# Kernel tuning notes

Hardware: AMD Instinct MI355X
Metric: run time of the kernel (lower is better)

## Reference

```python
import jax, jax.numpy as jnp
import numpy as np

B, C_IN, C_OUT = 2, 32, 32
N_IN = 128 * 128            # input grid points
N_OUT = 128 * 128           # output grid points
KERNEL_SIZE = 9             # (3-1)*4 + 1 for kernel_shape=[3,4], piecewise_linear basis
NNZ = 1_500_000             # sparse entries in psi (kernel_size, n_out, n_in)


def setup_inputs() -> dict:
    key = jax.random.key(0)
    ks = jax.random.split(key, 8)
    scale = (1.0 / C_IN) ** 0.5  # sqrt(1/groupsize), groups=1
    return {
        "x": jax.random.normal(ks[0], (B, C_IN, N_IN), jnp.float32),
        "quadrature_weights": jax.random.uniform(ks[1], (N_IN,), jnp.float32, 0.5, 1.5) / N_IN,
        "psi_vals": jax.random.uniform(ks[2], (NNZ,), jnp.float32),
        "weight": scale * jax.random.normal(ks[3], (C_OUT, C_IN, KERNEL_SIZE), jnp.float32),
        "bias": jnp.zeros((C_OUT,), jnp.float32),
        "psi_idx_k": jax.random.randint(ks[4], (NNZ,), 0, KERNEL_SIZE, dtype=jnp.int32),
        "psi_idx_out": jax.random.randint(ks[5], (NNZ,), 0, N_OUT, dtype=jnp.int32),
        "psi_idx_in": jax.random.randint(ks[6], (NNZ,), 0, N_IN, dtype=jnp.int32),
        "n_out": N_OUT,
    }


def reference(x, quadrature_weights, psi_vals, weight, bias,
              psi_idx_k, psi_idx_out, psi_idx_in, n_out):
    # x: (B, C, n_in); weight: (O, C, K); psi is sparse (K, n_out, n_in)
    Bb, C, n_in = x.shape
    K = weight.shape[2]
    # pre-multiply by quadrature weights, layout (n_in, B, C) for gather
    xq = (x * quadrature_weights[None, None, :]).transpose(2, 0, 1)
    # gather-weight: contribution of each sparse entry  -> (nnz, B, C)
    contrib = xq[psi_idx_in] * psi_vals[:, None, None]
    # scatter-add into (kernel, out) bins == sparse psi @ xq
    seg = psi_idx_k * n_out + psi_idx_out
    xk = jax.ops.segment_sum(contrib, seg, num_segments=K * n_out)
    xk = xk.reshape(K, n_out, Bb, C)  # (K, n_out, B, C)
    # channel/kernel mixing with learned weight (groups=1)
    out = jnp.einsum("knbc,ock->bon", xk, weight) + bias[None, :, None]
    return out  # (B, out_channels, n_out)
```

## Files before the change

kernel.cpp:

```cpp
#include <hip/hip_runtime.h>

#define N_IN   16384
#define N_OUT  16384
#define KSZ    9
#define CIN    32
#define COUT   32
#define BC     64
#define NCB    256
#define CHA    4096
#define ECAP_A 8192
#define ROWS   144
#define XSTR   68
#define SCAP   2048

union PrepSH {
    struct { int cnt[NCB]; int cntE[NCB]; int gbase[NCB]; int cursor[NCB];
             float2 slist[CHA]; } bin;
    struct { float tile[64 * 65]; } xqp;
};

__global__ __launch_bounds__(512) void k_prep(
        const float* __restrict__ x, const float* __restrict__ qw,
        const float* __restrict__ vals, const float* __restrict__ w,
        const int* __restrict__ ik, const int* __restrict__ io,
        const int* __restrict__ ii, float* __restrict__ xq,
        float2* __restrict__ sivA, int* __restrict__ gcntA,
        float* __restrict__ wT, int nnz, int nchA) {
    __shared__ PrepSH sh;
    const int t = threadIdx.x;
    const int bid = blockIdx.x;

    if (bid >= nchA) {
        if (bid < nchA + 256) {
            const int in0 = (bid - nchA) * 64;
#pragma unroll
            for (int i = 0; i < 8; ++i) {
                int idx = t + i * 512;
                int bcl = idx >> 6, inl = idx & 63;
                sh.xqp.tile[bcl * 65 + inl] = x[bcl * N_IN + in0 + inl];
            }
            __syncthreads();
#pragma unroll
            for (int i = 0; i < 8; ++i) {
                int idx = t + i * 512;
                int inl = idx >> 6, bcl = idx & 63;
                xq[(size_t)(in0 + inl) * BC + bcl] = sh.xqp.tile[bcl * 65 + inl] * qw[in0 + inl];
            }
        } else {
            for (int i = t; i < COUT * CIN * KSZ; i += 512) {
                int o = i / (CIN * KSZ);
                int r = i - o * (CIN * KSZ);
                int c = r / KSZ;
                int k = r - c * KSZ;
                wT[((k * 8 + (o >> 2)) * 32 + c) * 4 + (o & 3)] = w[i];
            }
        }
        return;
    }

    if (t < NCB) sh.bin.cnt[t] = 0;
    __syncthreads();
    const int base = bid * CHA;
    const int e0   = base + t * 8;

    float vv[8]; int pk[8]; int bk[8]; bool hv[8];
    if (e0 + 8 <= nnz) {
        int4 a0 = *(const int4*)(io + e0),  a1 = *(const int4*)(io + e0 + 4);
        int4 b0 = *(const int4*)(ii + e0),  b1 = *(const int4*)(ii + e0 + 4);
        int4 k0 = *(const int4*)(ik + e0),  k1 = *(const int4*)(ik + e0 + 4);
        float4 d0 = *(const float4*)(vals + e0), d1 = *(const float4*)(vals + e0 + 4);
        int ov[8] = {a0.x, a0.y, a0.z, a0.w, a1.x, a1.y, a1.z, a1.w};
        int iv[8] = {b0.x, b0.y, b0.z, b0.w, b1.x, b1.y, b1.z, b1.w};
        int kv[8] = {k0.x, k0.y, k0.z, k0.w, k1.x, k1.y, k1.z, k1.w};
        float dv[8] = {d0.x, d0.y, d0.z, d0.w, d1.x, d1.y, d1.z, d1.w};
#pragma unroll
        for (int j = 0; j < 8; ++j) {
            hv[j] = true;
            bk[j] = ov[j] >> 6;
            pk[j] = (int)(((unsigned)(ov[j] >> 4) << 22)) | (iv[j] << 8) | (kv[j] * 16 + (ov[j] & 15));
            vv[j] = dv[j];
        }
    } else {
#pragma unroll
        for (int j = 0; j < 8; ++j) {
            int e = e0 + j;
            hv[j] = (e < nnz);
            if (hv[j]) {
                int o = io[e];
                bk[j] = o >> 6;
                pk[j] = (int)(((unsigned)(o >> 4) << 22)) | (ii[e] << 8) | (ik[e] * 16 + (o & 15));
                vv[j] = vals[e];
            } else { bk[j] = 0; pk[j] = 0; vv[j] = 0.f; }
        }
    }
#pragma unroll
    for (int j = 0; j < 8; ++j) if (hv[j]) atomicAdd(&sh.bin.cnt[bk[j]], 1);
    __syncthreads();
    if (t < NCB) {
        int cv = sh.bin.cnt[t];
        sh.bin.gbase[t] = t * ECAP_A + (cv ? atomicAdd(&gcntA[t], cv) : 0);
    }
    if (t < 64) {
        int carry = 0;
#pragma unroll
        for (int seg = 0; seg < 4; ++seg) {
            int idx = seg * 64 + t;
            int v = sh.bin.cnt[idx];
            int orig = v;
#pragma unroll
            for (int off = 1; off < 64; off <<= 1) {
                int u = __shfl_up(v, off);
                if (t >= off) v += u;
            }
            sh.bin.cntE[idx]   = carry + v - orig;
            sh.bin.cursor[idx] = carry + v - orig;
            carry += __shfl(v, 63);
        }
    }
    __syncthreads();
#pragma unroll
    for (int j = 0; j < 8; ++j) {
        if (hv[j]) {
            int pos = atomicAdd(&sh.bin.cursor[bk[j]], 1);
            sh.bin.slist[pos] = make_float2(vv[j], __int_as_float(pk[j]));
        }
    }
    __syncthreads();
    const int m = min(nnz - base, CHA);
    for (int p = t; p < m; p += 512) {
        float2 f2 = sh.bin.slist[p];
        int cb = (int)((unsigned)__float_as_int(f2.y) >> 24);
        int dest = sh.bin.gbase[cb] + (p - sh.bin.cntE[cb]);
        if (dest < (cb + 1) * ECAP_A) sivA[dest] = f2;
    }
}

__global__ __launch_bounds__(512) void k_fused6(const float* __restrict__ xq,
        const float2* __restrict__ sivA, const int* __restrict__ gcntA,
        const float* __restrict__ wT, const float* __restrict__ bias,
        float* __restrict__ out) {
    __shared__ __align__(16) float sxk[80 * XSTR];
    __shared__ float2 slist[SCAP];
    __shared__ int    rowStart[ROWS + 1];
    __shared__ int    cursor[ROWS];
    __shared__ int    mcur;
    const int tid  = threadIdx.x;
    const int lane = tid & 63;
    const int wv   = __builtin_amdgcn_readfirstlane(tid >> 6);
    const unsigned f = blockIdx.x;

    if (tid < ROWS) rowStart[tid] = 0;
    if (tid == 0) mcur = 0;
    __syncthreads();

    const int cb = (int)(f >> 2);
    const int mA = min(gcntA[cb], ECAP_A);
    const float2* src = sivA + (size_t)cb * ECAP_A;
    float2* tmp = (float2*)sxk;
    for (int i = tid; i < mA; i += 512) {
        float2 v = src[i];
        unsigned fid = (unsigned)__float_as_int(v.y) >> 22;
        if (fid == f) {
            int pos = atomicAdd(&mcur, 1);
            if (pos < SCAP) {
                tmp[pos] = v;
                atomicAdd(&rowStart[__float_as_int(v.y) & 0xFF], 1);
            }
        }
    }
    __syncthreads();
    const int m2 = min(mcur, SCAP);
    if (wv == 0) {
        int carry = 0;
#pragma unroll
        for (int i0 = 0; i0 < 192; i0 += 64) {
            int idx = i0 + lane;
            int v = (idx < ROWS) ? rowStart[idx] : 0;
            int orig = v;
#pragma unroll
            for (int off = 1; off < 64; off <<= 1) {
                int u = __shfl_up(v, off);
                if (lane >= off) v += u;
            }
            if (idx < ROWS) {
                int excl = carry + v - orig;
                rowStart[idx] = excl;
                cursor[idx]   = excl;
            }
            carry += __shfl(v, 63);
        }
        if (lane == 0) rowStart[ROWS] = carry;
    }
    __syncthreads();
    for (int i = tid; i < m2; i += 512) {
        float2 v = tmp[i];
        int p = __float_as_int(v.y);
        int pos = atomicAdd(&cursor[p & 0xFF], 1);
        slist[pos] = make_float2(v.x, __int_as_float(p & 0x3FFF00));
    }
    __syncthreads();

    const char* xqb   = (const char*)xq;
    const int   lane4 = lane * 4;
    const int   h     = lane >> 4;
    const int   nl    = lane & 15;
    float acc[4] = {0.f, 0.f, 0.f, 0.f};

#pragma unroll
    for (int ph = 0; ph < 2; ++ph) {
        const int rbase = ph ? 80 : 0;
        const int rend  = ph ? 144 : 80;
        const int nrows = rend - rbase;
        for (int i = tid; i < nrows * XSTR; i += 512) sxk[i] = 0.f;
        __syncthreads();
        for (int r = rbase + wv; r < rend; r += 8) {
            const int a = rowStart[r], b = rowStart[r + 1];
            if (a >= b) continue;
            float acc0 = 0.f, acc1 = 0.f, acc2 = 0.f, acc3 = 0.f;
            int i = a;
            for (; i + 7 < b; i += 8) {
                float2 v0 = slist[i],     v1 = slist[i + 1], v2 = slist[i + 2], v3 = slist[i + 3];
                float2 v4 = slist[i + 4], v5 = slist[i + 5], v6 = slist[i + 6], v7 = slist[i + 7];
                acc0 += *(const float*)(xqb + (__float_as_int(v0.y) + lane4)) * v0.x;
                acc1 += *(const float*)(xqb + (__float_as_int(v1.y) + lane4)) * v1.x;
                acc2 += *(const float*)(xqb + (__float_as_int(v2.y) + lane4)) * v2.x;
                acc3 += *(const float*)(xqb + (__float_as_int(v3.y) + lane4)) * v3.x;
                acc0 += *(const float*)(xqb + (__float_as_int(v4.y) + lane4)) * v4.x;
                acc1 += *(const float*)(xqb + (__float_as_int(v5.y) + lane4)) * v5.x;
                acc2 += *(const float*)(xqb + (__float_as_int(v6.y) + lane4)) * v6.x;
                acc3 += *(const float*)(xqb + (__float_as_int(v7.y) + lane4)) * v7.x;
            }
            for (; i + 3 < b; i += 4) {
                float2 v0 = slist[i], v1 = slist[i + 1], v2 = slist[i + 2], v3 = slist[i + 3];
                acc0 += *(const float*)(xqb + (__float_as_int(v0.y) + lane4)) * v0.x;
                acc1 += *(const float*)(xqb + (__float_as_int(v1.y) + lane4)) * v1.x;
                acc2 += *(const float*)(xqb + (__float_as_int(v2.y) + lane4)) * v2.x;
                acc3 += *(const float*)(xqb + (__float_as_int(v3.y) + lane4)) * v3.x;
            }
            for (; i < b; ++i) {
                float2 v = slist[i];
                acc0 += *(const float*)(xqb + (__float_as_int(v.y) + lane4)) * v.x;
            }
            sxk[(r - rbase) * XSTR + lane] = (acc0 + acc1) + (acc2 + acc3);
        }
        __syncthreads();
        if (lane < 32) {
            const int kbase = ph ? 5 : 0;
            const int kcnt  = ph ? 4 : 5;
            for (int kk = 0; kk < kcnt; ++kk) {
                const float* xr = &sxk[(kk * 16 + nl) * XSTR + h * 32];
                const float* wp = &wT[((kbase + kk) * 8 + wv) * 128];
#pragma unroll
                for (int c4 = 0; c4 < 8; ++c4) {
                    float4 xv = *(const float4*)&xr[c4 * 4];
#pragma unroll
                    for (int cc = 0; cc < 4; ++cc) {
                        float xval = (&xv.x)[cc];
#pragma unroll
                        for (int j = 0; j < 4; ++j)
                            acc[j] += xval * wp[(c4 * 4 + cc) * 4 + j];
                    }
                }
            }
        }
        __syncthreads();
    }

    if (lane < 32) {
        const int n0 = (int)f * 16;
#pragma unroll
        for (int j = 0; j < 4; ++j) {
            int o = wv * 4 + j;
            out[((size_t)h * COUT + o) * N_OUT + n0 + nl] = acc[j] + bias[o];
        }
    }
}

extern "C" void kernel_launch(void* const* d_in, const int* in_sizes, int n_in,
                              void* d_out, int out_size, void* d_ws, size_t ws_size,
                              hipStream_t stream) {
    const float* x    = (const float*)d_in[0];
    const float* qw   = (const float*)d_in[1];
    const float* vals = (const float*)d_in[2];
    const float* w    = (const float*)d_in[3];
    const float* bias = (const float*)d_in[4];
    const int*   ik   = (const int*)d_in[5];
    const int*   io   = (const int*)d_in[6];
    const int*   ii   = (const int*)d_in[7];
    const int    nnz  = in_sizes[2];
    const int    nchA = (nnz + CHA - 1) / CHA;

    char* ws = (char*)d_ws;
    float*  xq    = (float*)ws;  ws += (size_t)N_IN * BC * 4;
    float2* sivA  = (float2*)ws; ws += (size_t)NCB * ECAP_A * 8;
    int*    gcntA = (int*)ws;    ws += NCB * 4;
    float*  wT    = (float*)ws;  ws += (size_t)COUT * CIN * KSZ * 4;

    hipMemsetAsync(gcntA, 0, NCB * sizeof(int), stream);
    k_prep  <<<nchA + 257, 512, 0, stream>>>(x, qw, vals, w, ik, io, ii,
                                             xq, sivA, gcntA, wT, nnz, nchA);
    k_fused6<<<1024, 512, 0, stream>>>(xq, sivA, gcntA, wT, bias, (float*)d_out);
}
```

Measured before the change: 149.2 us.

## Bin sparse entries directly per 32-output tile and use 1024-thread fused blocks

The prep kernel now bins entries into 512 buckets of 32 output points each, so every fused block reads only its own bucket. Before, four blocks each scanned a shared 64-point bucket and filtered out the entries that were not theirs. The fused kernel runs 512 blocks of 1024 threads, processes 288 rows in three phases of 96, and splits the channel-mixing work across all 16 waves. The aim is to remove the redundant bucket scanning and the temporary compaction pass, and to keep more lanes busy during mixing. The trade-off is fewer blocks overall and tighter capacity clamping per bucket (4096 entries, against an average of about 2900).

After: 297.8 us. 2x slower.

```diff
diff --git a/kernel.cpp b/kernel.cpp
--- a/kernel.cpp
+++ b/kernel.cpp
@@ -6,16 +6,16 @@
 #define CIN    32
 #define COUT   32
 #define BC     64
-#define NCB    256
+#define NCB    512
 #define CHA    4096
-#define ECAP_A 8192
-#define ROWS   144
+#define ECAP_F 4096
+#define ROWS   288
+#define PHROWS 96
 #define XSTR   68
-#define SCAP   2048
 
 union PrepSH {
     struct { int cnt[NCB]; int cntE[NCB]; int gbase[NCB]; int cursor[NCB];
-             float2 slist[CHA]; } bin;
+             int segsum[8]; float2 slist[CHA]; } bin;
     struct { float tile[64 * 65]; } xqp;
 };
 
@@ -24,7 +24,7 @@
         const float* __restrict__ vals, const float* __restrict__ w,
         const int* __restrict__ ik, const int* __restrict__ io,
         const int* __restrict__ ii, float* __restrict__ xq,
-        float2* __restrict__ sivA, int* __restrict__ gcntA,
+        float2* __restrict__ sivF, int* __restrict__ gcntF,
         float* __restrict__ wT, int nnz, int nchA) {
     __shared__ PrepSH sh;
     const int t = threadIdx.x;
@@ -58,7 +58,7 @@
         return;
     }
 
-    if (t < NCB) sh.bin.cnt[t] = 0;
+    sh.bin.cnt[t] = 0;
     __syncthreads();
     const int base = bid * CHA;
     const int e0   = base + t * 8;
@@ -76,8 +76,8 @@
 #pragma unroll
         for (int j = 0; j < 8; ++j) {
             hv[j] = true;
-            bk[j] = ov[j] >> 6;
-            pk[j] = (int)(((unsigned)(ov[j] >> 4) << 22)) | (iv[j] << 8) | (kv[j] * 16 + (ov[j] & 15));
+            bk[j] = ov[j] >> 5;
+            pk[j] = (int)(((unsigned)(ov[j] >> 5)) << 23) | (iv[j] << 9) | (kv[j] * 32 + (ov[j] & 31));
             vv[j] = dv[j];
         }
     } else {
@@ -87,8 +87,8 @@
             hv[j] = (e < nnz);
             if (hv[j]) {
                 int o = io[e];
-                bk[j] = o >> 6;
-                pk[j] = (int)(((unsigned)(o >> 4) << 22)) | (ii[e] << 8) | (ik[e] * 16 + (o & 15));
+                bk[j] = o >> 5;
+                pk[j] = (int)(((unsigned)(o >> 5)) << 23) | (ii[e] << 9) | (ik[e] * 32 + (o & 31));
                 vv[j] = vals[e];
             } else { bk[j] = 0; pk[j] = 0; vv[j] = 0.f; }
         }
@@ -96,27 +96,28 @@
 #pragma unroll
     for (int j = 0; j < 8; ++j) if (hv[j]) atomicAdd(&sh.bin.cnt[bk[j]], 1);
     __syncthreads();
-    if (t < NCB) {
-        int cv = sh.bin.cnt[t];
-        sh.bin.gbase[t] = t * ECAP_A + (cv ? atomicAdd(&gcntA[t], cv) : 0);
-    }
-    if (t < 64) {
-        int carry = 0;
-#pragma unroll
-        for (int seg = 0; seg < 4; ++seg) {
-            int idx = seg * 64 + t;
-            int v = sh.bin.cnt[idx];
-            int orig = v;
-#pragma unroll
-            for (int off = 1; off < 64; off <<= 1) {
-                int u = __shfl_up(v, off);
-                if (t >= off) v += u;
-            }
-            sh.bin.cntE[idx]   = carry + v - orig;
-            sh.bin.cursor[idx] = carry + v - orig;
-            carry += __shfl(v, 63);
-        }
-    }
+
+    const int lane = t & 63;
+    const int wvp  = t >> 6;
+    const int cv = sh.bin.cnt[t];
+    sh.bin.gbase[t] = t * ECAP_F + (cv ? atomicAdd(&gcntF[t], cv) : 0);
+    int v = cv;
+#pragma unroll
+    for (int off = 1; off < 64; off <<= 1) {
+        int u = __shfl_up(v, off);
+        if (lane >= off) v += u;
+    }
+    if (lane == 63) sh.bin.segsum[wvp] = v;
+    __syncthreads();
+    if (t == 0) {
+        int c = 0;
+#pragma unroll
+        for (int s = 0; s < 8; ++s) { int xs = sh.bin.segsum[s]; sh.bin.segsum[s] = c; c += xs; }
+    }
+    __syncthreads();
+    const int excl = v - cv + sh.bin.segsum[wvp];
+    sh.bin.cntE[t]   = excl;
+    sh.bin.cursor[t] = excl;
     __syncthreads();
 #pragma unroll
     for (int j = 0; j < 8; ++j) {
@@ -129,51 +130,39 @@
     const int m = min(nnz - base, CHA);
     for (int p = t; p < m; p += 512) {
         float2 f2 = sh.bin.slist[p];
-        int cb = (int)((unsigned)__float_as_int(f2.y) >> 24);
+        int cb = (int)((unsigned)__float_as_int(f2.y) >> 23);
         int dest = sh.bin.gbase[cb] + (p - sh.bin.cntE[cb]);
-        if (dest < (cb + 1) * ECAP_A) sivA[dest] = f2;
+        if (dest < (cb + 1) * ECAP_F) sivF[dest] = f2;
     }
 }
 
-__global__ __launch_bounds__(512) void k_fused6(const float* __restrict__ xq,
-        const float2* __restrict__ sivA, const int* __restrict__ gcntA,
+__global__ __launch_bounds__(1024, 8) void k_fused7(const float* __restrict__ xq,
+        const float2* __restrict__ sivF, const int* __restrict__ gcntF,
         const float* __restrict__ wT, const float* __restrict__ bias,
         float* __restrict__ out) {
-    __shared__ __align__(16) float sxk[80 * XSTR];
-    __shared__ float2 slist[SCAP];
-    __shared__ int    rowStart[ROWS + 1];
-    __shared__ int    cursor[ROWS];
-    __shared__ int    mcur;
+    __shared__ __align__(16) float sxk[PHROWS * XSTR];
+    __shared__ __align__(16) float2 slist[ECAP_F];
+    __shared__ int rowStart[ROWS + 1];
+    __shared__ int cursor[ROWS];
     const int tid  = threadIdx.x;
     const int lane = tid & 63;
     const int wv   = __builtin_amdgcn_readfirstlane(tid >> 6);
     const unsigned f = blockIdx.x;
 
     if (tid < ROWS) rowStart[tid] = 0;
-    if (tid == 0) mcur = 0;
-    __syncthreads();
-
-    const int cb = (int)(f >> 2);
-    const int mA = min(gcntA[cb], ECAP_A);
-    const float2* src = sivA + (size_t)cb * ECAP_A;
-    float2* tmp = (float2*)sxk;
-    for (int i = tid; i < mA; i += 512) {
-        float2 v = src[i];
-        unsigned fid = (unsigned)__float_as_int(v.y) >> 22;
-        if (fid == f) {
-            int pos = atomicAdd(&mcur, 1);
-            if (pos < SCAP) {
-                tmp[pos] = v;
-                atomicAdd(&rowStart[__float_as_int(v.y) & 0xFF], 1);
-            }
-        }
-    }
-    __syncthreads();
-    const int m2 = min(mcur, SCAP);
+    __syncthreads();
+
+    const int mF = min(gcntF[f], ECAP_F);
+    const float2* __restrict__ src = sivF + (size_t)f * ECAP_F;
+    const int* __restrict__ srcI = (const int*)src;
+    for (int i = tid; i < mF; i += 1024)
+        atomicAdd(&rowStart[srcI[2 * i + 1] & 0x1FF], 1);
+    __syncthreads();
+
     if (wv == 0) {
         int carry = 0;
 #pragma unroll
-        for (int i0 = 0; i0 < 192; i0 += 64) {
+        for (int i0 = 0; i0 < 320; i0 += 64) {
             int idx = i0 + lane;
             int v = (idx < ROWS) ? rowStart[idx] : 0;
             int orig = v;
@@ -192,30 +181,28 @@
         if (lane == 0) rowStart[ROWS] = carry;
     }
     __syncthreads();
-    for (int i = tid; i < m2; i += 512) {
-        float2 v = tmp[i];
+
+    for (int i = tid; i < mF; i += 1024) {
+        float2 v = src[i];
         int p = __float_as_int(v.y);
-        int pos = atomicAdd(&cursor[p & 0xFF], 1);
-        slist[pos] = make_float2(v.x, __int_as_float(p & 0x3FFF00));
+        int pos = atomicAdd(&cursor[p & 0x1FF], 1);
+        slist[pos] = make_float2(v.x, __int_as_float((p >> 1) & 0x3FFF00));
     }
     __syncthreads();
 
     const char* xqb   = (const char*)xq;
     const int   lane4 = lane * 4;
-    const int   h     = lane >> 4;
-    const int   nl    = lane & 15;
-    float acc[4] = {0.f, 0.f, 0.f, 0.f};
-
-#pragma unroll
-    for (int ph = 0; ph < 2; ++ph) {
-        const int rbase = ph ? 80 : 0;
-        const int rend  = ph ? 144 : 80;
-        const int nrows = rend - rbase;
-        for (int i = tid; i < nrows * XSTR; i += 512) sxk[i] = 0.f;
-        __syncthreads();
-        for (int r = rbase + wv; r < rend; r += 8) {
+    const int   b_    = lane >> 5;
+    const int   n32   = lane & 31;
+    const int   oq    = wv >> 1;
+    const int   ol    = (wv & 1) * 2;
+    float acc[2] = {0.f, 0.f};
+
+#pragma unroll
+    for (int ph = 0; ph < 3; ++ph) {
+        const int rbase = ph * PHROWS;
+        for (int r = rbase + wv; r < rbase + PHROWS; r += 16) {
             const int a = rowStart[r], b = rowStart[r + 1];
-            if (a >= b) continue;
             float acc0 = 0.f, acc1 = 0.f, acc2 = 0.f, acc3 = 0.f;
             int i = a;
             for (; i + 7 < b; i += 8) {
@@ -244,35 +231,30 @@
             sxk[(r - rbase) * XSTR + lane] = (acc0 + acc1) + (acc2 + acc3);
         }
         __syncthreads();
-        if (lane < 32) {
-            const int kbase = ph ? 5 : 0;
-            const int kcnt  = ph ? 4 : 5;
-            for (int kk = 0; kk < kcnt; ++kk) {
-                const float* xr = &sxk[(kk * 16 + nl) * XSTR + h * 32];
-                const float* wp = &wT[((kbase + kk) * 8 + wv) * 128];
-#pragma unroll
-                for (int c4 = 0; c4 < 8; ++c4) {
-                    float4 xv = *(const float4*)&xr[c4 * 4];
-#pragma unroll
-                    for (int cc = 0; cc < 4; ++cc) {
-                        float xval = (&xv.x)[cc];
-#pragma unroll
-                        for (int j = 0; j < 4; ++j)
-                            acc[j] += xval * wp[(c4 * 4 + cc) * 4 + j];
-                    }
+        const int kbase = ph * 3;
+#pragma unroll
+        for (int kk = 0; kk < 3; ++kk) {
+            const float* xr = &sxk[(kk * 32 + n32) * XSTR + b_ * 32];
+            const float* wp = &wT[((kbase + kk) * 8 + oq) * 128 + ol];
+#pragma unroll
+            for (int c4 = 0; c4 < 8; ++c4) {
+                float4 xv = *(const float4*)&xr[c4 * 4];
+#pragma unroll
+                for (int cc = 0; cc < 4; ++cc) {
+                    float xval = (&xv.x)[cc];
+                    acc[0] += xval * wp[(c4 * 4 + cc) * 4];
+                    acc[1] += xval * wp[(c4 * 4 + cc) * 4 + 1];
                 }
             }
         }
         __syncthreads();
     }
 
-    if (lane < 32) {
-        const int n0 = (int)f * 16;
-#pragma unroll
-        for (int j = 0; j < 4; ++j) {
-            int o = wv * 4 + j;
-            out[((size_t)h * COUT + o) * N_OUT + n0 + nl] = acc[j] + bias[o];
-        }
+    const int n0 = (int)f * 32;
+#pragma unroll
+    for (int j = 0; j < 2; ++j) {
+        int o = oq * 4 + ol + j;
+        out[((size_t)b_ * COUT + o) * N_OUT + n0 + n32] = acc[j] + bias[o];
     }
 }
 
@@ -292,12 +274,12 @@
 
     char* ws = (char*)d_ws;
     float*  xq    = (float*)ws;  ws += (size_t)N_IN * BC * 4;
-    float2* sivA  = (float2*)ws; ws += (size_t)NCB * ECAP_A * 8;
-    int*    gcntA = (int*)ws;    ws += NCB * 4;
+    float2* sivF  = (float2*)ws; ws += (size_t)NCB * ECAP_F * 8;
+    int*    gcntF = (int*)ws;    ws += NCB * 4;
     float*  wT    = (float*)ws;  ws += (size_t)COUT * CIN * KSZ * 4;
 
-    hipMemsetAsync(gcntA, 0, NCB * sizeof(int), stream);
+    hipMemsetAsync(gcntF, 0, NCB * sizeof(int), stream);
     k_prep  <<<nchA + 257, 512, 0, stream>>>(x, qw, vals, w, ik, io, ii,
-                                             xq, sivA, gcntA, wT, nnz, nchA);
-    k_fused6<<<1024, 512, 0, stream>>>(xq, sivA, gcntA, wT, bias, (float*)d_out);
+                                             xq, sivF, gcntF, wT, nnz, nchA);
+    k_fused7<<<NCB, 1024, 0, stream>>>(xq, sivF, gcntF, wT, bias, (float*)d_out);
 }
```

## Bin sparse entries directly per output block to skip second-stage filtering

Applied to the files above, without the earlier changes.

The prep kernel now buckets entries into 1024 fine bins, one per consumer block, instead of 256 coarse bins. Each fused block therefore reads only its own entries. Before, it scanned a whole coarse bin of about 4x more data and filtered by block id with a shared atomic cursor. The global bin counters are padded with a stride of 16 to spread atomic contention. This trades a larger shared-memory histogram and a two-level scan in prep for a cheaper fused kernel, and it uses a tighter per-bin capacity that overflow could exceed.

Result: slower. 174.0 us (+16.7%).

```diff
diff --git a/kernel.cpp b/kernel.cpp
--- a/kernel.cpp
+++ b/kernel.cpp
@@ -6,16 +6,16 @@
 #define CIN    32
 #define COUT   32
 #define BC     64
-#define NCB    256
+#define NCB    1024
 #define CHA    4096
-#define ECAP_A 8192
+#define ECAP_F 2048
+#define GSTR   16
 #define ROWS   144
 #define XSTR   68
-#define SCAP   2048
 
 union PrepSH {
     struct { int cnt[NCB]; int cntE[NCB]; int gbase[NCB]; int cursor[NCB];
-             float2 slist[CHA]; } bin;
+             int segsum[8]; float2 slist[CHA]; } bin;
     struct { float tile[64 * 65]; } xqp;
 };
 
@@ -24,7 +24,7 @@
         const float* __restrict__ vals, const float* __restrict__ w,
         const int* __restrict__ ik, const int* __restrict__ io,
         const int* __restrict__ ii, float* __restrict__ xq,
-        float2* __restrict__ sivA, int* __restrict__ gcntA,
+        float2* __restrict__ sivF, int* __restrict__ gcntF,
         float* __restrict__ wT, int nnz, int nchA) {
     __shared__ PrepSH sh;
     const int t = threadIdx.x;
@@ -58,7 +58,8 @@
         return;
     }
 
-    if (t < NCB) sh.bin.cnt[t] = 0;
+    sh.bin.cnt[t] = 0;
+    sh.bin.cnt[t + 512] = 0;
     __syncthreads();
     const int base = bid * CHA;
     const int e0   = base + t * 8;
@@ -76,7 +77,7 @@
 #pragma unroll
         for (int j = 0; j < 8; ++j) {
             hv[j] = true;
-            bk[j] = ov[j] >> 6;
+            bk[j] = ov[j] >> 4;
             pk[j] = (int)(((unsigned)(ov[j] >> 4) << 22)) | (iv[j] << 8) | (kv[j] * 16 + (ov[j] & 15));
             vv[j] = dv[j];
         }
@@ -87,7 +88,7 @@
             hv[j] = (e < nnz);
             if (hv[j]) {
                 int o = io[e];
-                bk[j] = o >> 6;
+                bk[j] = o >> 4;
                 pk[j] = (int)(((unsigned)(o >> 4) << 22)) | (ii[e] << 8) | (ik[e] * 16 + (o & 15));
                 vv[j] = vals[e];
             } else { bk[j] = 0; pk[j] = 0; vv[j] = 0.f; }
@@ -96,26 +97,42 @@
 #pragma unroll
     for (int j = 0; j < 8; ++j) if (hv[j]) atomicAdd(&sh.bin.cnt[bk[j]], 1);
     __syncthreads();
-    if (t < NCB) {
-        int cv = sh.bin.cnt[t];
-        sh.bin.gbase[t] = t * ECAP_A + (cv ? atomicAdd(&gcntA[t], cv) : 0);
-    }
-    if (t < 64) {
+
+    const int lane = t & 63;
+    const int wvp  = t >> 6;
+    int cvv[2], exclv[2];
+    {
         int carry = 0;
 #pragma unroll
-        for (int seg = 0; seg < 4; ++seg) {
-            int idx = seg * 64 + t;
-            int v = sh.bin.cnt[idx];
-            int orig = v;
+        for (int s = 0; s < 2; ++s) {
+            const int idx = wvp * 128 + s * 64 + lane;
+            const int cv = sh.bin.cnt[idx];
+            cvv[s] = cv;
+            sh.bin.gbase[idx] = idx * ECAP_F + (cv ? atomicAdd(&gcntF[idx * GSTR], cv) : 0);
+            int v = cv;
 #pragma unroll
             for (int off = 1; off < 64; off <<= 1) {
                 int u = __shfl_up(v, off);
-                if (t >= off) v += u;
-            }
-            sh.bin.cntE[idx]   = carry + v - orig;
-            sh.bin.cursor[idx] = carry + v - orig;
+                if (lane >= off) v += u;
+            }
+            exclv[s] = carry + v - cv;
             carry += __shfl(v, 63);
         }
+        if (lane == 0) sh.bin.segsum[wvp] = carry;
+    }
+    __syncthreads();
+    if (t == 0) {
+        int c = 0;
+#pragma unroll
+        for (int s = 0; s < 8; ++s) { int xs = sh.bin.segsum[s]; sh.bin.segsum[s] = c; c += xs; }
+    }
+    __syncthreads();
+#pragma unroll
+    for (int s = 0; s < 2; ++s) {
+        const int idx = wvp * 128 + s * 64 + lane;
+        const int e = exclv[s] + sh.bin.segsum[wvp];
+        sh.bin.cntE[idx]   = e;
+        sh.bin.cursor[idx] = e;
     }
     __syncthreads();
 #pragma unroll
@@ -129,47 +146,35 @@
     const int m = min(nnz - base, CHA);
     for (int p = t; p < m; p += 512) {
         float2 f2 = sh.bin.slist[p];
-        int cb = (int)((unsigned)__float_as_int(f2.y) >> 24);
+        int cb = (int)((unsigned)__float_as_int(f2.y) >> 22);
         int dest = sh.bin.gbase[cb] + (p - sh.bin.cntE[cb]);
-        if (dest < (cb + 1) * ECAP_A) sivA[dest] = f2;
+        if (dest < (cb + 1) * ECAP_F) sivF[dest] = f2;
     }
 }
 
-__global__ __launch_bounds__(512) void k_fused6(const float* __restrict__ xq,
-        const float2* __restrict__ sivA, const int* __restrict__ gcntA,
+__global__ __launch_bounds__(512) void k_fused8(const float* __restrict__ xq,
+        const float2* __restrict__ sivF, const int* __restrict__ gcntF,
         const float* __restrict__ wT, const float* __restrict__ bias,
         float* __restrict__ out) {
     __shared__ __align__(16) float sxk[80 * XSTR];
-    __shared__ float2 slist[SCAP];
+    __shared__ __align__(16) float2 slist[ECAP_F];
     __shared__ int    rowStart[ROWS + 1];
     __shared__ int    cursor[ROWS];
-    __shared__ int    mcur;
     const int tid  = threadIdx.x;
     const int lane = tid & 63;
     const int wv   = __builtin_amdgcn_readfirstlane(tid >> 6);
     const unsigned f = blockIdx.x;
 
     if (tid < ROWS) rowStart[tid] = 0;
-    if (tid == 0) mcur = 0;
-    __syncthreads();
-
-    const int cb = (int)(f >> 2);
-    const int mA = min(gcntA[cb], ECAP_A);
-    const float2* src = sivA + (size_t)cb * ECAP_A;
-    float2* tmp = (float2*)sxk;
-    for (int i = tid; i < mA; i += 512) {
-        float2 v = src[i];
-        unsigned fid = (unsigned)__float_as_int(v.y) >> 22;
-        if (fid == f) {
-            int pos = atomicAdd(&mcur, 1);
-            if (pos < SCAP) {
-                tmp[pos] = v;
-                atomicAdd(&rowStart[__float_as_int(v.y) & 0xFF], 1);
-            }
-        }
-    }
-    __syncthreads();
-    const int m2 = min(mcur, SCAP);
+    __syncthreads();
+
+    const int mF = min(gcntF[f * GSTR], ECAP_F);
+    const float2* __restrict__ src = sivF + (size_t)f * ECAP_F;
+    const int* __restrict__ srcI = (const int*)src;
+    for (int i = tid; i < mF; i += 512)
+        atomicAdd(&rowStart[srcI[2 * i + 1] & 0xFF], 1);
+    __syncthreads();
+
     if (wv == 0) {
         int carry = 0;
 #pragma unroll
@@ -192,8 +197,8 @@
         if (lane == 0) rowStart[ROWS] = carry;
     }
     __syncthreads();
-    for (int i = tid; i < m2; i += 512) {
-        float2 v = tmp[i];
+    for (int i = tid; i < mF; i += 512) {
+        float2 v = src[i];
         int p = __float_as_int(v.y);
         int pos = atomicAdd(&cursor[p & 0xFF], 1);
         slist[pos] = make_float2(v.x, __int_as_float(p & 0x3FFF00));
@@ -292,12 +297,12 @@
 
     char* ws = (char*)d_ws;
     float*  xq    = (float*)ws;  ws += (size_t)N_IN * BC * 4;
-    float2* sivA  = (float2*)ws; ws += (size_t)NCB * ECAP_A * 8;
-    int*    gcntA = (int*)ws;    ws += NCB * 4;
+    float2* sivF  = (float2*)ws; ws += (size_t)NCB * ECAP_F * 8;
+    int*    gcntF = (int*)ws;    ws += (size_t)NCB * GSTR * 4;
     float*  wT    = (float*)ws;  ws += (size_t)COUT * CIN * KSZ * 4;
 
-    hipMemsetAsync(gcntA, 0, NCB * sizeof(int), stream);
+    hipMemsetAsync(gcntF, 0, (size_t)NCB * GSTR * sizeof(int), stream);
     k_prep  <<<nchA + 257, 512, 0, stream>>>(x, qw, vals, w, ik, io, ii,
-                                             xq, sivA, gcntA, wT, nnz, nchA);
-    k_fused6<<<1024, 512, 0, stream>>>(xq, sivA, gcntA, wT, bias, (float*)d_out);
+                                             xq, sivF, gcntF, wT, nnz, nchA);
+    k_fused8<<<NCB, 512, 0, stream>>>(xq, sivF, gcntF, wT, bias, (float*)d_out);
 }
```

## Merge four output-tile blocks per bin and overlap gather with mixing via double buffering

Applied to the files above, without the earlier changes.

The second kernel now launches one 1024-thread block per coarse bin instead of four 512-thread blocks that each rescanned the same bin's entries. Each entry is read once, kept in registers, bucketed by tile and row, and sorted into a larger shared list, which removes the redundant global reads and filtering. Work is then split across waves: half the waves gather the next half-tile of rows into one of two shared buffers while the other half run the channel/kernel mixing on the current buffer. In exchange the grid shrinks to 256 blocks, which may underfill the GPU, and shared memory per block grows substantially.

Result: slower. 177.2 us (+18.8%).

```diff
diff --git a/kernel.cpp b/kernel.cpp
--- a/kernel.cpp
+++ b/kernel.cpp
@@ -9,9 +9,8 @@
 #define NCB    256
 #define CHA    4096
 #define ECAP_A 8192
-#define ROWS   144
+#define ROWS4  576
 #define XSTR   68
-#define SCAP   2048
 
 union PrepSH {
     struct { int cnt[NCB]; int cntE[NCB]; int gbase[NCB]; int cursor[NCB];
@@ -135,68 +134,68 @@
     }
 }
 
-__global__ __launch_bounds__(512) void k_fused6(const float* __restrict__ xq,
+__global__ __launch_bounds__(1024) void k_fused10(const float* __restrict__ xq,
         const float2* __restrict__ sivA, const int* __restrict__ gcntA,
         const float* __restrict__ wT, const float* __restrict__ bias,
         float* __restrict__ out) {
-    __shared__ __align__(16) float sxk[80 * XSTR];
-    __shared__ float2 slist[SCAP];
-    __shared__ int    rowStart[ROWS + 1];
-    __shared__ int    cursor[ROWS];
-    __shared__ int    mcur;
+    __shared__ __align__(16) float sxk[2 * 80 * XSTR];
+    __shared__ __align__(16) float2 slist[ECAP_A];
+    __shared__ int rowStart[ROWS4 + 1];
+    __shared__ int cursor[ROWS4];
     const int tid  = threadIdx.x;
     const int lane = tid & 63;
     const int wv   = __builtin_amdgcn_readfirstlane(tid >> 6);
-    const unsigned f = blockIdx.x;
-
-    if (tid < ROWS) rowStart[tid] = 0;
-    if (tid == 0) mcur = 0;
-    __syncthreads();
-
-    const int cb = (int)(f >> 2);
+    const int cb   = blockIdx.x;
+
+    for (int i = tid; i < ROWS4; i += 1024) rowStart[i] = 0;
+    __syncthreads();
+
     const int mA = min(gcntA[cb], ECAP_A);
-    const float2* src = sivA + (size_t)cb * ECAP_A;
-    float2* tmp = (float2*)sxk;
-    for (int i = tid; i < mA; i += 512) {
-        float2 v = src[i];
-        unsigned fid = (unsigned)__float_as_int(v.y) >> 22;
-        if (fid == f) {
-            int pos = atomicAdd(&mcur, 1);
-            if (pos < SCAP) {
-                tmp[pos] = v;
-                atomicAdd(&rowStart[__float_as_int(v.y) & 0xFF], 1);
-            }
-        }
-    }
-    __syncthreads();
-    const int m2 = min(mcur, SCAP);
+    const float2* __restrict__ src = sivA + (size_t)cb * ECAP_A;
+
+    float2 rv[8];
+#pragma unroll
+    for (int j = 0; j < 8; ++j) {
+        const int i = tid + j * 1024;
+        if (i < mA) {
+            float2 v = src[i];
+            rv[j] = v;
+            int p = __float_as_int(v.y);
+            atomicAdd(&rowStart[((p >> 22) & 3) * 144 + (p & 0xFF)], 1);
+        }
+    }
+    __syncthreads();
+
     if (wv == 0) {
         int carry = 0;
 #pragma unroll
-        for (int i0 = 0; i0 < 192; i0 += 64) {
-            int idx = i0 + lane;
-            int v = (idx < ROWS) ? rowStart[idx] : 0;
+        for (int seg = 0; seg < 9; ++seg) {
+            int idx = seg * 64 + lane;
+            int v = rowStart[idx];
             int orig = v;
 #pragma unroll
             for (int off = 1; off < 64; off <<= 1) {
                 int u = __shfl_up(v, off);
                 if (lane >= off) v += u;
             }
-            if (idx < ROWS) {
-                int excl = carry + v - orig;
-                rowStart[idx] = excl;
-                cursor[idx]   = excl;
-            }
+            int excl = carry + v - orig;
+            rowStart[idx] = excl;
+            cursor[idx]   = excl;
             carry += __shfl(v, 63);
         }
-        if (lane == 0) rowStart[ROWS] = carry;
-    }
-    __syncthreads();
-    for (int i = tid; i < m2; i += 512) {
-        float2 v = tmp[i];
-        int p = __float_as_int(v.y);
-        int pos = atomicAdd(&cursor[p & 0xFF], 1);
-        slist[pos] = make_float2(v.x, __int_as_float(p & 0x3FFF00));
+        if (lane == 0) rowStart[ROWS4] = carry;
+    }
+    __syncthreads();
+
+#pragma unroll
+    for (int j = 0; j < 8; ++j) {
+        const int i = tid + j * 1024;
+        if (i < mA) {
+            float2 v = rv[j];
+            int p = __float_as_int(v.y);
+            int pos = atomicAdd(&cursor[((p >> 22) & 3) * 144 + (p & 0xFF)], 1);
+            slist[pos] = make_float2(v.x, __int_as_float(p & 0x3FFF00));
+        }
     }
     __syncthreads();
 
@@ -206,49 +205,84 @@
     const int   nl    = lane & 15;
     float acc[4] = {0.f, 0.f, 0.f, 0.f};
 
-#pragma unroll
-    for (int ph = 0; ph < 2; ++ph) {
-        const int rbase = ph ? 80 : 0;
-        const int rend  = ph ? 144 : 80;
-        const int nrows = rend - rbase;
-        for (int i = tid; i < nrows * XSTR; i += 512) sxk[i] = 0.f;
-        __syncthreads();
-        for (int r = rbase + wv; r < rend; r += 8) {
-            const int a = rowStart[r], b = rowStart[r + 1];
-            if (a >= b) continue;
-            float acc0 = 0.f, acc1 = 0.f, acc2 = 0.f, acc3 = 0.f;
-            int i = a;
-            for (; i + 7 < b; i += 8) {
-                float2 v0 = slist[i],     v1 = slist[i + 1], v2 = slist[i + 2], v3 = slist[i + 3];
-                float2 v4 = slist[i + 4], v5 = slist[i + 5], v6 = slist[i + 6], v7 = slist[i + 7];
-                acc0 += *(const float*)(xqb + (__float_as_int(v0.y) + lane4)) * v0.x;
-                acc1 += *(const float*)(xqb + (__float_as_int(v1.y) + lane4)) * v1.x;
-                acc2 += *(const float*)(xqb + (__float_as_int(v2.y) + lane4)) * v2.x;
-                acc3 += *(const float*)(xqb + (__float_as_int(v3.y) + lane4)) * v3.x;
-                acc0 += *(const float*)(xqb + (__float_as_int(v4.y) + lane4)) * v4.x;
-                acc1 += *(const float*)(xqb + (__float_as_int(v5.y) + lane4)) * v5.x;
-                acc2 += *(const float*)(xqb + (__float_as_int(v6.y) + lane4)) * v6.x;
-                acc3 += *(const float*)(xqb + (__float_as_int(v7.y) + lane4)) * v7.x;
-            }
-            for (; i + 3 < b; i += 4) {
-                float2 v0 = slist[i], v1 = slist[i + 1], v2 = slist[i + 2], v3 = slist[i + 3];
-                acc0 += *(const float*)(xqb + (__float_as_int(v0.y) + lane4)) * v0.x;
-                acc1 += *(const float*)(xqb + (__float_as_int(v1.y) + lane4)) * v1.x;
-                acc2 += *(const float*)(xqb + (__float_as_int(v2.y) + lane4)) * v2.x;
-                acc3 += *(const float*)(xqb + (__float_as_int(v3.y) + lane4)) * v3.x;
-            }
-            for (; i < b; ++i) {
-                float2 v = slist[i];
-                acc0 += *(const float*)(xqb + (__float_as_int(v.y) + lane4)) * v.x;
-            }
-            sxk[(r - rbase) * XSTR + lane] = (acc0 + acc1) + (acc2 + acc3);
-        }
-        __syncthreads();
-        if (lane < 32) {
-            const int kbase = ph ? 5 : 0;
-            const int kcnt  = ph ? 4 : 5;
+    for (int r = wv; r < 80; r += 16) {
+        const int a = rowStart[r], b = rowStart[r + 1];
+        float acc0 = 0.f, acc1 = 0.f, acc2 = 0.f, acc3 = 0.f;
+        int i = a;
+        for (; i + 7 < b; i += 8) {
+            float2 v0 = slist[i],     v1 = slist[i + 1], v2 = slist[i + 2], v3 = slist[i + 3];
+            float2 v4 = slist[i + 4], v5 = slist[i + 5], v6 = slist[i + 6], v7 = slist[i + 7];
+            acc0 += *(const float*)(xqb + (__float_as_int(v0.y) + lane4)) * v0.x;
+            acc1 += *(const float*)(xqb + (__float_as_int(v1.y) + lane4)) * v1.x;
+            acc2 += *(const float*)(xqb + (__float_as_int(v2.y) + lane4)) * v2.x;
+            acc3 += *(const float*)(xqb + (__float_as_int(v3.y) + lane4)) * v3.x;
+            acc0 += *(const float*)(xqb + (__float_as_int(v4.y) + lane4)) * v4.x;
+            acc1 += *(const float*)(xqb + (__float_as_int(v5.y) + lane4)) * v5.x;
+            acc2 += *(const float*)(xqb + (__float_as_int(v6.y) + lane4)) * v6.x;
+            acc3 += *(const float*)(xqb + (__float_as_int(v7.y) + lane4)) * v7.x;
+        }
+        for (; i + 3 < b; i += 4) {
+            float2 v0 = slist[i], v1 = slist[i + 1], v2 = slist[i + 2], v3 = slist[i + 3];
+            acc0 += *(const float*)(xqb + (__float_as_int(v0.y) + lane4)) * v0.x;
+            acc1 += *(const float*)(xqb + (__float_as_int(v1.y) + lane4)) * v1.x;
+            acc2 += *(const float*)(xqb + (__float_as_int(v2.y) + lane4)) * v2.x;
+            acc3 += *(const float*)(xqb + (__float_as_int(v3.y) + lane4)) * v3.x;
+        }
+        for (; i < b; ++i) {
+            float2 v = slist[i];
+            acc0 += *(const float*)(xqb + (__float_as_int(v.y) + lane4)) * v.x;
+        }
+        sxk[r * XSTR + lane] = (acc0 + acc1) + (acc2 + acc3);
+    }
+    __syncthreads();
+
+#pragma unroll 1
+    for (int c = 0; c < 8; ++c) {
+        const int p = c & 1;
+        if (wv >= 8) {
+            if (c < 7) {
+                const int c2 = c + 1;
+                const int p2 = c2 & 1;
+                const int rb = (c2 >> 1) * 144 + (p2 ? 80 : 0);
+                const int nr = p2 ? 64 : 80;
+                float* buf = sxk + (c2 & 1) * (80 * XSTR);
+                for (int r0 = wv - 8; r0 < nr; r0 += 8) {
+                    const int r = rb + r0;
+                    const int a = rowStart[r], b = rowStart[r + 1];
+                    float acc0 = 0.f, acc1 = 0.f, acc2 = 0.f, acc3 = 0.f;
+                    int i = a;
+                    for (; i + 7 < b; i += 8) {
+                        float2 v0 = slist[i],     v1 = slist[i + 1], v2 = slist[i + 2], v3 = slist[i + 3];
+                        float2 v4 = slist[i + 4], v5 = slist[i + 5], v6 = slist[i + 6], v7 = slist[i + 7];
+                        acc0 += *(const float*)(xqb + (__float_as_int(v0.y) + lane4)) * v0.x;
+                        acc1 += *(const float*)(xqb + (__float_as_int(v1.y) + lane4)) * v1.x;
+                        acc2 += *(const float*)(xqb + (__float_as_int(v2.y) + lane4)) * v2.x;
+                        acc3 += *(const float*)(xqb + (__float_as_int(v3.y) + lane4)) * v3.x;
+                        acc0 += *(const float*)(xqb + (__float_as_int(v4.y) + lane4)) * v4.x;
+                        acc1 += *(const float*)(xqb + (__float_as_int(v5.y) + lane4)) * v5.x;
+                        acc2 += *(const float*)(xqb + (__float_as_int(v6.y) + lane4)) * v6.x;
+                        acc3 += *(const float*)(xqb + (__float_as_int(v7.y) + lane4)) * v7.x;
+                    }
+                    for (; i + 3 < b; i += 4) {
+                        float2 v0 = slist[i], v1 = slist[i + 1], v2 = slist[i + 2], v3 = slist[i + 3];
+                        acc0 += *(const float*)(xqb + (__float_as_int(v0.y) + lane4)) * v0.x;
+                        acc1 += *(const float*)(xqb + (__float_as_int(v1.y) + lane4)) * v1.x;
+                        acc2 += *(const float*)(xqb + (__float_as_int(v2.y) + lane4)) * v2.x;
+                        acc3 += *(const float*)(xqb + (__float_as_int(v3.y) + lane4)) * v3.x;
+                    }
+                    for (; i < b; ++i) {
+                        float2 v = slist[i];
+                        acc0 += *(const float*)(xqb + (__float_as_int(v.y) + lane4)) * v.x;
+                    }
+                    buf[r0 * XSTR + lane] = (acc0 + acc1) + (acc2 + acc3);
+                }
+            }
+        } else if (lane < 32) {
+            const float* buf = sxk + (c & 1) * (80 * XSTR);
+            const int kbase = p ? 5 : 0;
+            const int kcnt  = p ? 4 : 5;
             for (int kk = 0; kk < kcnt; ++kk) {
-                const float* xr = &sxk[(kk * 16 + nl) * XSTR + h * 32];
+                const float* xr = &buf[(kk * 16 + nl) * XSTR + h * 32];
                 const float* wp = &wT[((kbase + kk) * 8 + wv) * 128];
 #pragma unroll
                 for (int c4 = 0; c4 < 8; ++c4) {
@@ -262,17 +296,17 @@
                     }
                 }
             }
+            if (p == 1) {
+                const int n0 = (cb * 4 + (c >> 1)) * 16;
+#pragma unroll
+                for (int j = 0; j < 4; ++j) {
+                    int o = wv * 4 + j;
+                    out[((size_t)h * COUT + o) * N_OUT + n0 + nl] = acc[j] + bias[o];
+                    acc[j] = 0.f;
+                }
+            }
         }
         __syncthreads();
-    }
-
-    if (lane < 32) {
-        const int n0 = (int)f * 16;
-#pragma unroll
-        for (int j = 0; j < 4; ++j) {
-            int o = wv * 4 + j;
-            out[((size_t)h * COUT + o) * N_OUT + n0 + nl] = acc[j] + bias[o];
-        }
     }
 }
 
@@ -297,7 +331,7 @@
     float*  wT    = (float*)ws;  ws += (size_t)COUT * CIN * KSZ * 4;
 
     hipMemsetAsync(gcntA, 0, NCB * sizeof(int), stream);
-    k_prep  <<<nchA + 257, 512, 0, stream>>>(x, qw, vals, w, ik, io, ii,
-                                             xq, sivA, gcntA, wT, nnz, nchA);
-    k_fused6<<<1024, 512, 0, stream>>>(xq, sivA, gcntA, wT, bias, (float*)d_out);
+    k_prep   <<<nchA + 257, 512, 0, stream>>>(x, qw, vals, w, ik, io, ii,
+                                              xq, sivA, gcntA, wT, nnz, nchA);
+    k_fused10<<<NCB, 1024, 0, stream>>>(xq, sivA, gcntA, wT, bias, (float*)d_out);
 }
```
